# Kernel tuning notes

Hardware: AMD Instinct MI355X
Metric: run time of the kernel (lower is better)

The kernel has to match this reference:

```python
import jax, jax.numpy as jnp
import numpy as np

B, C, H, W = 8, 256, 128, 128
KC, VC, HEADS = 256, 256, 8


def setup_inputs() -> dict:
    key = jax.random.key(0)
    ks = jax.random.split(key, 10)
    s = 0.05
    return {
        "x": jax.random.normal(ks[0], (B, C, H, W), jnp.float32),
        "Wk": jax.random.normal(ks[1], (KC, C), jnp.float32) * s,
        "bk": jax.random.normal(ks[2], (KC,), jnp.float32) * s,
        "Wq": jax.random.normal(ks[3], (KC, C), jnp.float32) * s,
        "bq": jax.random.normal(ks[4], (KC,), jnp.float32) * s,
        "Wv": jax.random.normal(ks[5], (VC, C), jnp.float32) * s,
        "bv": jax.random.normal(ks[6], (VC,), jnp.float32) * s,
        "Wr": jax.random.normal(ks[7], (C, VC), jnp.float32) * s,
        "br": jax.random.normal(ks[8], (C,), jnp.float32) * s,
        "head_count": HEADS,
    }


def reference(x, Wk, bk, Wq, bq, Wv, bv, Wr, br, head_count):
    n, c, h, w = x.shape
    hw = h * w
    xf = x.reshape(n, c, hw)  # [n, C, S]
    # 1x1 convs == per-pixel linear projections
    keys = jnp.einsum('kc,ncs->nks', Wk, xf) + bk[None, :, None]
    queries = jnp.einsum('kc,ncs->nks', Wq, xf) + bq[None, :, None]
    values = jnp.einsum('vc,ncs->nvs', Wv, xf) + bv[None, :, None]

    dk = Wk.shape[0] // head_count
    dv = Wv.shape[0] // head_count
    # split heads along channel dim (matches torch channel slicing)
    K = jax.nn.softmax(keys.reshape(n, head_count, dk, hw), axis=-1)   # softmax over spatial
    Q = jax.nn.softmax(queries.reshape(n, head_count, dk, hw), axis=2) # softmax over key dim
    V = values.reshape(n, head_count, dv, hw)

    # context = K @ V^T : [n, h, dk, dv]
    ctx = jnp.einsum('nhks,nhvs->nhkv', K, V)
    # attended = ctx^T @ Q : [n, h, dv, S]
    att = jnp.einsum('nhkv,nhks->nhvs', ctx, Q).reshape(n, head_count * dv, h, w)

    attention = jnp.einsum('ov,nvhw->nohw', Wr, att) + br[None, :, None, None]
    # attention map: per-head mean over key dim, then mean over heads
    attention_map = K.mean(axis=2).mean(axis=1).reshape(n, h, w)
    # torch returns the LAST head's context (loop variable after the loop)
    context_last = ctx[:, -1]
    return attention, context_last, attention_map
```

## Files before the change

kernel.cpp:

```cpp
#include <hip/hip_runtime.h>
#include <hip/hip_bf16.h>

typedef float f32x4 __attribute__((ext_vector_type(4)));
typedef short s16x8 __attribute__((ext_vector_type(8)));
typedef short s16x4 __attribute__((ext_vector_type(4)));
typedef __bf16 bf16x8 __attribute__((ext_vector_type(8)));
typedef unsigned short u16;

#define DEVI __device__ __forceinline__

static constexpr int    HW      = 16384;
static constexpr size_t BSTRIDE = (size_t)256 * HW;

static constexpr size_t oXBT   = 0;
static constexpr size_t oEK    = oXBT  + (size_t)8 * HW * 256 * 2;
static constexpr size_t oQT    = oEK   + (size_t)8 * 256 * HW * 2;
static constexpr size_t oVB    = oQT   + (size_t)8 * HW * 256 * 2;
static constexpr size_t oWK    = oVB   + (size_t)8 * 256 * HW * 2;
static constexpr size_t oBIAS  = oWK   + (size_t)768 * 256 * 2;
static constexpr size_t oISE   = oBIAS + 4096;
static constexpr size_t oPS    = oISE  + 8192;
static constexpr size_t oCTX   = oPS   + (size_t)256 * 2048 * 4;
static constexpr size_t oMB    = oCTX  + (size_t)64 * 1024 * 4;
static constexpr size_t oCPART = oMB   + (size_t)8 * 256 * 256 * 2;
static constexpr size_t oMPART = oCPART + (size_t)4096 * 1024 * 4;

DEVI float bf2f(short x) {
  unsigned u = ((unsigned)(unsigned short)x) << 16;
  return __builtin_bit_cast(float, u);
}
DEVI u16 f2bf(float x) { return __builtin_bit_cast(u16, (__bf16)x); }

DEVI void gld16(const void* g, void* l) {
  __builtin_amdgcn_global_load_lds(
      (__attribute__((address_space(1))) void*)(g),
      (__attribute__((address_space(3))) void*)(l), 16, 0, 0);
}

DEVI void cfence() { asm volatile("" ::: "memory"); }

__global__ __launch_bounds__(256) void k_prep(
    const float* __restrict__ Wk, const float* __restrict__ Wq, const float* __restrict__ Wv,
    const float* __restrict__ bk, const float* __restrict__ bq, const float* __restrict__ bv,
    u16* __restrict__ Wkqv, float* __restrict__ bias)
{
  int i = blockIdx.x * 256 + threadIdx.x;
  for (int p = i; p < 768 * 256; p += 64 * 256) {
    float v = (p < 65536) ? Wk[p] : (p < 131072 ? Wq[p - 65536] : Wv[p - 131072]);
    Wkqv[p] = f2bf(v);
  }
  if (i < 768) bias[i] = (i < 256) ? bk[i] : (i < 512 ? bq[i - 256] : bv[i - 512]);
}

__global__ __launch_bounds__(256) void k_transpose(const float* __restrict__ in_, u16* __restrict__ out)
{
  __shared__ u16 lds[64 * 256];
  const int t = threadIdx.x;
  const int n = blockIdx.y;
  const int s0 = blockIdx.x * 64;
  const float* src = in_ + ((size_t)n * 256 + t) * HW + s0;
  #pragma unroll
  for (int i = 0; i < 16; ++i) {
    f32x4 v = *(const f32x4*)(src + i * 4);
    #pragma unroll
    for (int j = 0; j < 4; ++j) lds[(i * 4 + j) * 256 + t] = f2bf(v[j]);
  }
  __syncthreads();
  s16x8* gp = (s16x8*)(out + (size_t)n * BSTRIDE + (size_t)s0 * 256);
  const s16x8* lp = (const s16x8*)lds;
  #pragma unroll
  for (int i = 0; i < 8; ++i) gp[t + i * 256] = lp[t + i * 256];
}

template<int MODE>
__global__ __launch_bounds__(512, 2) void k_gemm256(
    const u16* __restrict__ A, const u16* __restrict__ B, const float* __restrict__ bias,
    u16* __restrict__ o_ek, u16* __restrict__ o_qT, u16* __restrict__ o_vb,
    float* __restrict__ o_ps, float* __restrict__ o_f32)
{
  __shared__ u16 smem[65536];
  const int t = threadIdx.x;
  const int L = blockIdx.x;
  const int n = L & 7;
  const int idx = L >> 3;
  int mb, sb;
  if constexpr (MODE == 0) { mb = idx % 3; sb = idx / 3; }
  else                     { mb = 0;       sb = idx; }
  const int s0 = sb * 256;
  const int lane = t & 63;
  const int l15 = lane & 15, l4 = lane >> 4;
  const int w = t >> 6;
  const int wr = w & 1, wc = w >> 1;
  const int tr = t >> 3;
  const int csw = (t & 7) ^ (tr & 7);

  const u16* Ag = A + (MODE == 0 ? (size_t)mb * 65536 : (size_t)n * 65536);
  const u16* Bg = B + (size_t)n * BSTRIDE + (size_t)s0 * 256;

  auto STAGE = [&](int buf, int kt) {
    const int k0 = kt * 64 + csw * 8;
    #pragma unroll
    for (int i = 0; i < 4; ++i) {
      const size_t r = (size_t)(i * 64 + tr);
      gld16(Ag + r * 256 + k0, smem + buf * 16384 + (i * 512 + t) * 8);
      gld16(Bg + r * 256 + k0, smem + 32768 + buf * 16384 + (i * 512 + t) * 8);
    }
  };

  f32x4 acc[8][4] = {};

  auto COMPUTE = [&](int buf) {
    const u16* Al = smem + buf * 16384;
    const u16* Bl = smem + 32768 + buf * 16384;
    bf16x8 bf[4][2];
    #pragma unroll
    for (int b = 0; b < 4; ++b) {
      const int s = wc * 64 + b * 16 + l15;
      #pragma unroll
      for (int ks = 0; ks < 2; ++ks)
        bf[b][ks] = *(const bf16x8*)&Bl[s * 64 + ((ks * 4 + l4) ^ (s & 7)) * 8];
    }
    #pragma unroll
    for (int p = 0; p < 4; ++p) {
      bf16x8 af[2][2];
      #pragma unroll
      for (int a2 = 0; a2 < 2; ++a2) {
        const int m = wr * 128 + (p * 2 + a2) * 16 + l15;
        #pragma unroll
        for (int ks = 0; ks < 2; ++ks)
          af[a2][ks] = *(const bf16x8*)&Al[m * 64 + ((ks * 4 + l4) ^ (m & 7)) * 8];
      }
      __builtin_amdgcn_s_setprio(1);
      #pragma unroll
      for (int a2 = 0; a2 < 2; ++a2)
        #pragma unroll
        for (int b = 0; b < 4; ++b)
          #pragma unroll
          for (int ks = 0; ks < 2; ++ks)
            acc[p * 2 + a2][b] = __builtin_amdgcn_mfma_f32_16x16x32_bf16(
                af[a2][ks], bf[b][ks], acc[p * 2 + a2][b], 0, 0, 0);
      __builtin_amdgcn_s_setprio(0);
    }
  };

  STAGE(0, 0); STAGE(1, 1);
  #pragma unroll
  for (int kt = 0; kt < 4; ++kt) {
    if (kt < 3) asm volatile("s_waitcnt vmcnt(8)" ::: "memory");
    else        asm volatile("s_waitcnt vmcnt(0)" ::: "memory");
    cfence(); __builtin_amdgcn_s_barrier(); cfence();
    COMPUTE(kt & 1);
    asm volatile("s_waitcnt lgkmcnt(0)" ::: "memory");
    cfence(); __builtin_amdgcn_s_barrier(); cfence();
    if (kt < 2) STAGE(kt & 1, kt + 2);
  }
  __syncthreads();

  if constexpr (MODE == 1) {
    float* O = o_f32 + (size_t)n * BSTRIDE;
    #pragma unroll
    for (int am = 0; am < 8; ++am)
      #pragma unroll
      for (int r = 0; r < 4; ++r) {
        const int m = wr * 128 + am * 16 + l4 * 4 + r;
        const float bb = bias[m];
        float* op = O + (size_t)m * HW + s0 + wc * 64 + l15;
        #pragma unroll
        for (int b = 0; b < 4; ++b) op[b * 16] = acc[am][b][r] + bb;
      }
    return;
  } else {
  if (mb == 0) {
    float* psrow = o_ps + ((size_t)(sb * 4 + wc) * 8 + n) * 256;
    u16* O = o_ek + (size_t)n * BSTRIDE;
    #pragma unroll
    for (int am = 0; am < 8; ++am)
      #pragma unroll
      for (int r = 0; r < 4; ++r) {
        const int m = wr * 128 + am * 16 + l4 * 4 + r;
        const float bb = bias[m];
        const float e0 = __expf(acc[am][0][r] + bb), e1 = __expf(acc[am][1][r] + bb);
        const float e2 = __expf(acc[am][2][r] + bb), e3 = __expf(acc[am][3][r] + bb);
        float s_ = e0 + e1 + e2 + e3;
        s_ += __shfl_xor(s_, 1); s_ += __shfl_xor(s_, 2);
        s_ += __shfl_xor(s_, 4); s_ += __shfl_xor(s_, 8);
        if (l15 == 0) psrow[m] = s_;
        u16* op = O + (size_t)m * HW + s0 + wc * 64 + l15;
        op[0] = f2bf(e0); op[16] = f2bf(e1); op[32] = f2bf(e2); op[48] = f2bf(e3);
      }
  } else if (mb == 1) {
    #pragma unroll
    for (int am = 0; am < 8; ++am)
      #pragma unroll
      for (int r = 0; r < 4; ++r) {
        const float bb = bias[256 + wr * 128 + am * 16 + l4 * 4 + r];
        #pragma unroll
        for (int b = 0; b < 4; ++b) acc[am][b][r] += bb;
      }
    #pragma unroll
    for (int hh = 0; hh < 4; ++hh)
      #pragma unroll
      for (int b = 0; b < 4; ++b) {
        float s = 0.f;
        #pragma unroll
        for (int a2 = 0; a2 < 2; ++a2)
          #pragma unroll
          for (int r = 0; r < 4; ++r) {
            const float e = __expf(acc[hh * 2 + a2][b][r]);
            acc[hh * 2 + a2][b][r] = e; s += e;
          }
        s += __shfl_xor(s, 16); s += __shfl_xor(s, 32);
        const float inv = 1.f / s;
        #pragma unroll
        for (int a2 = 0; a2 < 2; ++a2)
          #pragma unroll
          for (int r = 0; r < 4; ++r) acc[hh * 2 + a2][b][r] *= inv;
      }
    #pragma unroll
    for (int H = 0; H < 2; ++H) {
      if ((wc >> 1) == H) {
        #pragma unroll
        for (int am = 0; am < 8; ++am)
          #pragma unroll
          for (int b = 0; b < 4; ++b) {
            const int srow = wc * 64 + b * 16 + l15 - H * 128;
            s16x4 pk;
            #pragma unroll
            for (int r = 0; r < 4; ++r) pk[r] = (short)f2bf(acc[am][b][r]);
            *(s16x4*)&smem[srow * 264 + wr * 128 + am * 16 + l4 * 4] = pk;
          }
      }
      __syncthreads();
      const int row = t >> 2;
      const int cq = (t & 3) * 64;
      u16* dst = o_qT + (size_t)n * BSTRIDE + (size_t)(s0 + H * 128 + row) * 256 + cq;
      const u16* srcl = smem + row * 264 + cq;
      #pragma unroll
      for (int i = 0; i < 8; ++i) *(s16x8*)(dst + i * 8) = *(const s16x8*)(srcl + i * 8);
      __syncthreads();
    }
  } else {
    u16* O = o_vb + (size_t)n * BSTRIDE;
    #pragma unroll
    for (int am = 0; am < 8; ++am)
      #pragma unroll
      for (int r = 0; r < 4; ++r) {
        const int m = wr * 128 + am * 16 + l4 * 4 + r;
        const float bb = bias[512 + m];
        u16* op = O + (size_t)m * HW + s0 + wc * 64 + l15;
        #pragma unroll
        for (int b = 0; b < 4; ++b) op[b * 16] = f2bf(acc[am][b][r] + bb);
      }
  }
  }
}

__global__ __launch_bounds__(256) void k_inv(const float* __restrict__ ps, float* __restrict__ ise)
{
  const int i = blockIdx.x * 256 + threadIdx.x;
  float s = 0.f;
  for (int b = 0; b < 256; ++b) s += ps[(size_t)b * 2048 + i];
  ise[i] = 1.f / s;
}

__global__ __launch_bounds__(64) void k_ctx_part(
    const u16* __restrict__ ek, const u16* __restrict__ vb, const float* __restrict__ ise,
    float* __restrict__ cpart, float* __restrict__ mpart)
{
  const int blk = blockIdx.x;
  const int chunk = blk & 63, nh = blk >> 6;
  const int h = nh & 7, n = nh >> 3;
  const int lane = threadIdx.x;
  const int l15 = lane & 15, l4 = lane >> 4;
  const u16* kb = ek + ((size_t)n * 256 + h * 32) * HW;
  const u16* vv = vb + ((size_t)n * 256 + h * 32) * HW;
  const float iv0 = ise[n * 256 + h * 32 + l15];
  const float iv1 = ise[n * 256 + h * 32 + 16 + l15];
  f32x4 acc[2][2] = {};
  float macc[8][8] = {};
  const int sbase = chunk * 256 + l4 * 8;
  #pragma unroll
  for (int ks = 0; ks < 8; ++ks) {
    const int sb = sbase + ks * 32;
    bf16x8 ef[2], vf[2];
    #pragma unroll
    for (int g = 0; g < 2; ++g) {
      ef[g] = *(const bf16x8*)(kb + (size_t)(g * 16 + l15) * HW + sb);
      vf[g] = *(const bf16x8*)(vv + (size_t)(g * 16 + l15) * HW + sb);
    }
    #pragma unroll
    for (int j = 0; j < 8; ++j)
      macc[ks][j] = fmaf(iv0, (float)ef[0][j], fmaf(iv1, (float)ef[1][j], macc[ks][j]));
    #pragma unroll
    for (int a = 0; a < 2; ++a)
      #pragma unroll
      for (int b = 0; b < 2; ++b)
        acc[a][b] = __builtin_amdgcn_mfma_f32_16x16x32_bf16(ef[a], vf[b], acc[a][b], 0, 0, 0);
  }
  float* op = cpart + (size_t)blk * 1024;
  #pragma unroll
  for (int a = 0; a < 2; ++a)
    #pragma unroll
    for (int b = 0; b < 2; ++b)
      #pragma unroll
      for (int r = 0; r < 4; ++r)
        op[(a * 16 + l4 * 4 + r) * 32 + b * 16 + l15] = acc[a][b][r];
  #pragma unroll
  for (int ks = 0; ks < 8; ++ks)
    #pragma unroll
    for (int j = 0; j < 8; ++j) {
      float v = macc[ks][j];
      v += __shfl_xor(v, 1); v += __shfl_xor(v, 2);
      v += __shfl_xor(v, 4); v += __shfl_xor(v, 8);
      macc[ks][j] = v;
    }
  if (l15 == 0) {
    float* mp = mpart + ((size_t)h * 8 + n) * HW + sbase;
    #pragma unroll
    for (int ks = 0; ks < 8; ++ks) {
      f32x4 a = {macc[ks][0], macc[ks][1], macc[ks][2], macc[ks][3]};
      f32x4 b = {macc[ks][4], macc[ks][5], macc[ks][6], macc[ks][7]};
      *(f32x4*)(mp + ks * 32)     = a;
      *(f32x4*)(mp + ks * 32 + 4) = b;
    }
  }
}

__global__ __launch_bounds__(256) void k_ctx_reduce(
    const float* __restrict__ cpart, const float* __restrict__ ise,
    float* __restrict__ ctx, float* __restrict__ dctx)
{
  const int nh = blockIdx.x, n = nh >> 3, h = nh & 7, t = threadIdx.x;
  f32x4 a = {};
  for (int c = 0; c < 64; ++c) a += *(const f32x4*)(cpart + ((size_t)nh * 64 + c) * 1024 + t * 4);
  const float inv = ise[n * 256 + h * 32 + (t >> 3)];
  a *= inv;
  *(f32x4*)(ctx + (size_t)nh * 1024 + t * 4) = a;
  if (h == 7) *(f32x4*)(dctx + (size_t)n * 1024 + t * 4) = a;
}

__global__ __launch_bounds__(256) void k_mmat(
    const float* __restrict__ ctx, const float* __restrict__ Wr, u16* __restrict__ Mb)
{
  const int nh = blockIdx.x, n = nh >> 3, h = nh & 7, o = threadIdx.x;
  __shared__ float cl[1024];
  #pragma unroll
  for (int i = 0; i < 4; ++i) cl[o + i * 256] = ctx[(size_t)nh * 1024 + o + i * 256];
  __syncthreads();
  float wr[32];
  const float* wp = Wr + (size_t)o * 256 + h * 32;
  #pragma unroll
  for (int v = 0; v < 32; ++v) wr[v] = wp[v];
  u16* mp = Mb + ((size_t)n * 256 + o) * 256 + h * 32;
  #pragma unroll 4
  for (int k = 0; k < 32; ++k) {
    float s = 0.f;
    #pragma unroll
    for (int v = 0; v < 32; ++v) s += wr[v] * cl[k * 32 + v];
    mp[k] = f2bf(s);
  }
}

__global__ __launch_bounds__(256) void k_map_reduce(const float* __restrict__ mpart, float* __restrict__ dmap)
{
  const int i = blockIdx.x * 256 + threadIdx.x;
  f32x4 a = {};
  #pragma unroll
  for (int h = 0; h < 8; ++h) a += *(const f32x4*)(mpart + (size_t)h * 131072 + (size_t)i * 4);
  a *= (1.0f / 256.0f);
  *(f32x4*)(dmap + (size_t)i * 4) = a;
}

extern "C" void kernel_launch(void* const* d_in, const int* in_sizes, int n_in,
                              void* d_out, int out_size, void* d_ws, size_t ws_size,
                              hipStream_t stream)
{
  (void)in_sizes; (void)n_in; (void)out_size; (void)ws_size;
  const float* x  = (const float*)d_in[0];
  const float* Wk = (const float*)d_in[1];
  const float* bk = (const float*)d_in[2];
  const float* Wq = (const float*)d_in[3];
  const float* bq = (const float*)d_in[4];
  const float* Wv = (const float*)d_in[5];
  const float* bv = (const float*)d_in[6];
  const float* Wr = (const float*)d_in[7];
  const float* br = (const float*)d_in[8];

  char* ws = (char*)d_ws;
  u16*   xbT  = (u16*)(ws + oXBT);
  u16*   ek   = (u16*)(ws + oEK);
  u16*   qT   = (u16*)(ws + oQT);
  u16*   vb   = (u16*)(ws + oVB);
  u16*   Wkqv = (u16*)(ws + oWK);
  float* bias = (float*)(ws + oBIAS);
  float* ise  = (float*)(ws + oISE);
  float* ps   = (float*)(ws + oPS);
  float* ctx  = (float*)(ws + oCTX);
  u16*   Mb   = (u16*)(ws + oMB);
  float* cpart= (float*)(ws + oCPART);
  float* mpart= (float*)(ws + oMPART);

  float* attn = (float*)d_out;
  float* dctx = (float*)d_out + 33554432;
  float* dmap = (float*)d_out + 33562624;

  k_prep<<<64, 256, 0, stream>>>(Wk, Wq, Wv, bk, bq, bv, Wkqv, bias);
  k_transpose<<<dim3(256, 8), 256, 0, stream>>>(x, xbT);
  k_gemm256<0><<<1536, 512, 0, stream>>>(Wkqv, xbT, bias, ek, qT, vb, ps, nullptr);
  k_inv<<<8, 256, 0, stream>>>(ps, ise);
  k_ctx_part<<<4096, 64, 0, stream>>>(ek, vb, ise, cpart, mpart);
  k_ctx_reduce<<<64, 256, 0, stream>>>(cpart, ise, ctx, dctx);
  k_mmat<<<64, 256, 0, stream>>>(ctx, Wr, Mb);
  k_map_reduce<<<128, 256, 0, stream>>>(mpart, dmap);
  k_gemm256<1><<<512, 512, 0, stream>>>(Mb, qT, br, nullptr, nullptr, nullptr, nullptr, attn);
}
```

Baseline: 316.6 us.

## Restructure projection GEMMs to keep weights in registers and stream spatial tiles

The 256x256 GEMM kernel is replaced by a 256-thread variant in which each wave holds its 64 rows of the weight matrix entirely in registers. Only 64-pixel B tiles are streamed through double-buffered LDS, and the epilogue runs per tile. The swapped MFMA operand order lets the ek, vb and attention outputs be written as vectorized 4-element stores, and the qT output is written directly without an LDS transpose. The transpose kernel also gets a padded LDS layout with a different thread mapping. The cost is high register pressure from the 32 resident A fragments, plus complex vmcnt accounting.

Measured after the change: 377.1 us. +19.1%, slower.

```diff
diff --git a/kernel.cpp b/kernel.cpp
--- a/kernel.cpp
+++ b/kernel.cpp
@@ -37,8 +37,6 @@
       (__attribute__((address_space(3))) void*)(l), 16, 0, 0);
 }
 
-DEVI void cfence() { asm volatile("" ::: "memory"); }
-
 __global__ __launch_bounds__(256) void k_prep(
     const float* __restrict__ Wk, const float* __restrict__ Wq, const float* __restrict__ Wv,
     const float* __restrict__ bk, const float* __restrict__ bq, const float* __restrict__ bv,
@@ -52,206 +50,217 @@
   if (i < 768) bias[i] = (i < 256) ? bk[i] : (i < 512 ? bq[i - 256] : bv[i - 512]);
 }
 
-__global__ __launch_bounds__(256) void k_transpose(const float* __restrict__ in_, u16* __restrict__ out)
-{
-  __shared__ u16 lds[64 * 256];
+__global__ __launch_bounds__(256) void k_transpose(const float* __restrict__ x, u16* __restrict__ out)
+{
+  __shared__ u16 T[64 * 264];
   const int t = threadIdx.x;
   const int n = blockIdx.y;
   const int s0 = blockIdx.x * 64;
-  const float* src = in_ + ((size_t)n * 256 + t) * HW + s0;
+  const int cg = t >> 4;
+  const int sl = (t & 15) * 4;
   #pragma unroll
   for (int i = 0; i < 16; ++i) {
-    f32x4 v = *(const f32x4*)(src + i * 4);
-    #pragma unroll
-    for (int j = 0; j < 4; ++j) lds[(i * 4 + j) * 256 + t] = f2bf(v[j]);
+    const int c = i * 16 + cg;
+    f32x4 v = *(const f32x4*)(x + ((size_t)n * 256 + c) * HW + s0 + sl);
+    #pragma unroll
+    for (int j = 0; j < 4; ++j) T[(sl + j) * 264 + c] = f2bf(v[j]);
   }
   __syncthreads();
-  s16x8* gp = (s16x8*)(out + (size_t)n * BSTRIDE + (size_t)s0 * 256);
-  const s16x8* lp = (const s16x8*)lds;
-  #pragma unroll
-  for (int i = 0; i < 8; ++i) gp[t + i * 256] = lp[t + i * 256];
+  const int sr = t >> 2, ch = (t & 3) * 64;
+  u16* dst = out + (size_t)n * BSTRIDE + (size_t)(s0 + sr) * 256 + ch;
+  const u16* srcl = &T[sr * 264 + ch];
+  #pragma unroll
+  for (int i = 0; i < 8; ++i) *(s16x8*)(dst + i * 8) = *(const s16x8*)(srcl + i * 8);
 }
 
 template<int MODE>
-__global__ __launch_bounds__(512, 2) void k_gemm256(
+__global__ __launch_bounds__(256, 2) void k_gemmT(
     const u16* __restrict__ A, const u16* __restrict__ B, const float* __restrict__ bias,
     u16* __restrict__ o_ek, u16* __restrict__ o_qT, u16* __restrict__ o_vb,
     float* __restrict__ o_ps, float* __restrict__ o_f32)
 {
-  __shared__ u16 smem[65536];
+  __shared__ u16 smem[32768];
   const int t = threadIdx.x;
   const int L = blockIdx.x;
   const int n = L & 7;
-  const int idx = L >> 3;
-  int mb, sb;
-  if constexpr (MODE == 0) { mb = idx % 3; sb = idx / 3; }
-  else                     { mb = 0;       sb = idx; }
-  const int s0 = sb * 256;
+  int mb, sblock;
+  if constexpr (MODE == 0) { const int idx = L >> 3; mb = idx % 3; sblock = idx / 3; }
+  else                     { mb = 0; sblock = L >> 3; }
   const int lane = t & 63;
-  const int l15 = lane & 15, l4 = lane >> 4;
+  const int l15 = lane & 15, l4 = (lane >> 4) & 3;
   const int w = t >> 6;
-  const int wr = w & 1, wc = w >> 1;
-  const int tr = t >> 3;
-  const int csw = (t & 7) ^ (tr & 7);
-
-  const u16* Ag = A + (MODE == 0 ? (size_t)mb * 65536 : (size_t)n * 65536);
-  const u16* Bg = B + (size_t)n * BSTRIDE + (size_t)s0 * 256;
-
-  auto STAGE = [&](int buf, int kt) {
-    const int k0 = kt * 64 + csw * 8;
-    #pragma unroll
-    for (int i = 0; i < 4; ++i) {
-      const size_t r = (size_t)(i * 64 + tr);
-      gld16(Ag + r * 256 + k0, smem + buf * 16384 + (i * 512 + t) * 8);
-      gld16(Bg + r * 256 + k0, smem + 32768 + buf * 16384 + (i * 512 + t) * 8);
+  const bool sw = (MODE == 1) || (mb != 1);
+
+  const u16* Ag = (MODE == 0) ? A + (size_t)mb * 65536 : A + (size_t)n * 65536;
+  const u16* Bg = B + (size_t)n * BSTRIDE;
+
+  bf16x8 af[4][8];
+  #pragma unroll
+  for (int mf = 0; mf < 4; ++mf)
+    #pragma unroll
+    for (int kc = 0; kc < 8; ++kc)
+      af[mf][kc] = *(const bf16x8*)(Ag + (size_t)(w * 64 + mf * 16 + l15) * 256 + kc * 32 + l4 * 8);
+
+  float biasv[4];
+  f32x4 bq[4];
+  if constexpr (MODE == 0) {
+    if (mb != 1) {
+      const int bb = (mb == 0) ? 0 : 512;
+      #pragma unroll
+      for (int mf = 0; mf < 4; ++mf) biasv[mf] = bias[bb + w * 64 + mf * 16 + l15];
+    } else {
+      #pragma unroll
+      for (int mf = 0; mf < 4; ++mf)
+        #pragma unroll
+        for (int r = 0; r < 4; ++r) bq[mf][r] = bias[256 + w * 64 + mf * 16 + l4 * 4 + r];
+    }
+  } else {
+    #pragma unroll
+    for (int mf = 0; mf < 4; ++mf) biasv[mf] = bias[w * 64 + mf * 16 + l15];
+  }
+
+  const int rl_base = w * 16;
+  auto STAGE = [&](int buf, int tile) {
+    const int s0t = (sblock * 4 + tile) * 64;
+    #pragma unroll
+    for (int i = 0; i < 8; ++i) {
+      const int rl = rl_base + i * 2 + (lane >> 5);
+      const size_t gsrc = (size_t)(s0t + rl) * 256 + (size_t)(((lane & 31) ^ (rl & 7)) * 8);
+      gld16(Bg + gsrc, smem + buf * 16384 + (rl_base + i * 2) * 256);
     }
   };
 
-  f32x4 acc[8][4] = {};
-
-  auto COMPUTE = [&](int buf) {
-    const u16* Al = smem + buf * 16384;
-    const u16* Bl = smem + 32768 + buf * 16384;
-    bf16x8 bf[4][2];
-    #pragma unroll
-    for (int b = 0; b < 4; ++b) {
-      const int s = wc * 64 + b * 16 + l15;
-      #pragma unroll
-      for (int ks = 0; ks < 2; ++ks)
-        bf[b][ks] = *(const bf16x8*)&Bl[s * 64 + ((ks * 4 + l4) ^ (s & 7)) * 8];
-    }
-    #pragma unroll
-    for (int p = 0; p < 4; ++p) {
-      bf16x8 af[2][2];
-      #pragma unroll
-      for (int a2 = 0; a2 < 2; ++a2) {
-        const int m = wr * 128 + (p * 2 + a2) * 16 + l15;
-        #pragma unroll
-        for (int ks = 0; ks < 2; ++ks)
-          af[a2][ks] = *(const bf16x8*)&Al[m * 64 + ((ks * 4 + l4) ^ (m & 7)) * 8];
+  STAGE(0, 0);
+  STAGE(1, 1);
+
+  u16* ekb = o_ek + (size_t)n * BSTRIDE;
+  u16* vbb = o_vb + (size_t)n * BSTRIDE;
+  u16* qtb = o_qT + (size_t)n * BSTRIDE;
+  float* ob = o_f32 + (size_t)n * BSTRIDE;
+
+  #pragma unroll
+  for (int st = 0; st < 4; ++st) {
+    if (st == 0)      asm volatile("s_waitcnt vmcnt(8)" ::: "memory");
+    else if (st == 1) asm volatile("s_waitcnt vmcnt(24)" ::: "memory");
+    else if (st == 2) asm volatile("s_waitcnt vmcnt(40)" ::: "memory");
+    else              asm volatile("s_waitcnt vmcnt(32)" ::: "memory");
+    __builtin_amdgcn_s_barrier();
+
+    const int buf = st & 1;
+    const u16* Bl = smem + buf * 16384;
+    f32x4 acc[4][4] = {};
+
+    if (sw) {
+      #pragma unroll
+      for (int kc = 0; kc < 8; ++kc) {
+        bf16x8 bf[4];
+        #pragma unroll
+        for (int sf = 0; sf < 4; ++sf)
+          bf[sf] = *(const bf16x8*)&Bl[(sf * 16 + l15) * 256 + (((kc * 4 + l4) ^ (l15 & 7)) * 8)];
+        __builtin_amdgcn_s_setprio(1);
+        #pragma unroll
+        for (int sf = 0; sf < 4; ++sf)
+          #pragma unroll
+          for (int mf = 0; mf < 4; ++mf)
+            acc[sf][mf] = __builtin_amdgcn_mfma_f32_16x16x32_bf16(bf[sf], af[mf][kc], acc[sf][mf], 0, 0, 0);
+        __builtin_amdgcn_s_setprio(0);
       }
-      __builtin_amdgcn_s_setprio(1);
-      #pragma unroll
-      for (int a2 = 0; a2 < 2; ++a2)
-        #pragma unroll
-        for (int b = 0; b < 4; ++b)
-          #pragma unroll
-          for (int ks = 0; ks < 2; ++ks)
-            acc[p * 2 + a2][b] = __builtin_amdgcn_mfma_f32_16x16x32_bf16(
-                af[a2][ks], bf[b][ks], acc[p * 2 + a2][b], 0, 0, 0);
-      __builtin_amdgcn_s_setprio(0);
-    }
-  };
-
-  STAGE(0, 0); STAGE(1, 1);
-  #pragma unroll
-  for (int kt = 0; kt < 4; ++kt) {
-    if (kt < 3) asm volatile("s_waitcnt vmcnt(8)" ::: "memory");
-    else        asm volatile("s_waitcnt vmcnt(0)" ::: "memory");
-    cfence(); __builtin_amdgcn_s_barrier(); cfence();
-    COMPUTE(kt & 1);
+    } else {
+      #pragma unroll
+      for (int kc = 0; kc < 8; ++kc) {
+        bf16x8 bf[4];
+        #pragma unroll
+        for (int sf = 0; sf < 4; ++sf)
+          bf[sf] = *(const bf16x8*)&Bl[(sf * 16 + l15) * 256 + (((kc * 4 + l4) ^ (l15 & 7)) * 8)];
+        __builtin_amdgcn_s_setprio(1);
+        #pragma unroll
+        for (int mf = 0; mf < 4; ++mf)
+          #pragma unroll
+          for (int sf = 0; sf < 4; ++sf)
+            acc[mf][sf] = __builtin_amdgcn_mfma_f32_16x16x32_bf16(af[mf][kc], bf[sf], acc[mf][sf], 0, 0, 0);
+        __builtin_amdgcn_s_setprio(0);
+      }
+    }
+
     asm volatile("s_waitcnt lgkmcnt(0)" ::: "memory");
-    cfence(); __builtin_amdgcn_s_barrier(); cfence();
-    if (kt < 2) STAGE(kt & 1, kt + 2);
-  }
-  __syncthreads();
-
-  if constexpr (MODE == 1) {
-    float* O = o_f32 + (size_t)n * BSTRIDE;
-    #pragma unroll
-    for (int am = 0; am < 8; ++am)
-      #pragma unroll
-      for (int r = 0; r < 4; ++r) {
-        const int m = wr * 128 + am * 16 + l4 * 4 + r;
-        const float bb = bias[m];
-        float* op = O + (size_t)m * HW + s0 + wc * 64 + l15;
-        #pragma unroll
-        for (int b = 0; b < 4; ++b) op[b * 16] = acc[am][b][r] + bb;
+    __builtin_amdgcn_s_barrier();
+    if (st < 2) STAGE(buf, st + 2);
+
+    const int s0t = (sblock * 4 + st) * 64;
+    if constexpr (MODE == 1) {
+      #pragma unroll
+      for (int sf = 0; sf < 4; ++sf)
+        #pragma unroll
+        for (int mf = 0; mf < 4; ++mf) {
+          f32x4 o = acc[sf][mf] + biasv[mf];
+          __builtin_nontemporal_store(
+              o, (f32x4*)(ob + (size_t)(w * 64 + mf * 16 + l15) * HW + s0t + sf * 16 + l4 * 4));
+        }
+    } else if (mb == 0) {
+      float prow[4] = {0.f, 0.f, 0.f, 0.f};
+      #pragma unroll
+      for (int sf = 0; sf < 4; ++sf)
+        #pragma unroll
+        for (int mf = 0; mf < 4; ++mf) {
+          f32x4 e;
+          #pragma unroll
+          for (int r = 0; r < 4; ++r) e[r] = __expf(acc[sf][mf][r] + biasv[mf]);
+          prow[mf] += e[0] + e[1] + e[2] + e[3];
+          s16x4 pk;
+          #pragma unroll
+          for (int r = 0; r < 4; ++r) pk[r] = (short)f2bf(e[r]);
+          *(s16x4*)(ekb + (size_t)(w * 64 + mf * 16 + l15) * HW + s0t + sf * 16 + l4 * 4) = pk;
+        }
+      const int stile = sblock * 4 + st;
+      #pragma unroll
+      for (int mf = 0; mf < 4; ++mf) {
+        float v = prow[mf];
+        v += __shfl_xor(v, 16); v += __shfl_xor(v, 32);
+        prow[mf] = v;
       }
-    return;
-  } else {
-  if (mb == 0) {
-    float* psrow = o_ps + ((size_t)(sb * 4 + wc) * 8 + n) * 256;
-    u16* O = o_ek + (size_t)n * BSTRIDE;
-    #pragma unroll
-    for (int am = 0; am < 8; ++am)
-      #pragma unroll
-      for (int r = 0; r < 4; ++r) {
-        const int m = wr * 128 + am * 16 + l4 * 4 + r;
-        const float bb = bias[m];
-        const float e0 = __expf(acc[am][0][r] + bb), e1 = __expf(acc[am][1][r] + bb);
-        const float e2 = __expf(acc[am][2][r] + bb), e3 = __expf(acc[am][3][r] + bb);
-        float s_ = e0 + e1 + e2 + e3;
-        s_ += __shfl_xor(s_, 1); s_ += __shfl_xor(s_, 2);
-        s_ += __shfl_xor(s_, 4); s_ += __shfl_xor(s_, 8);
-        if (l15 == 0) psrow[m] = s_;
-        u16* op = O + (size_t)m * HW + s0 + wc * 64 + l15;
-        op[0] = f2bf(e0); op[16] = f2bf(e1); op[32] = f2bf(e2); op[48] = f2bf(e3);
+      if (l4 == 0) {
+        #pragma unroll
+        for (int mf = 0; mf < 4; ++mf)
+          o_ps[(size_t)stile * 2048 + n * 256 + w * 64 + mf * 16 + l15] = prow[mf];
       }
-  } else if (mb == 1) {
-    #pragma unroll
-    for (int am = 0; am < 8; ++am)
-      #pragma unroll
-      for (int r = 0; r < 4; ++r) {
-        const float bb = bias[256 + wr * 128 + am * 16 + l4 * 4 + r];
-        #pragma unroll
-        for (int b = 0; b < 4; ++b) acc[am][b][r] += bb;
+    } else if (mb == 1) {
+      #pragma unroll
+      for (int mf = 0; mf < 4; ++mf)
+        #pragma unroll
+        for (int sf = 0; sf < 4; ++sf)
+          #pragma unroll
+          for (int r = 0; r < 4; ++r) acc[mf][sf][r] = __expf(acc[mf][sf][r] + bq[mf][r]);
+      #pragma unroll
+      for (int sf = 0; sf < 4; ++sf) {
+        float h0 = 0.f, h1 = 0.f;
+        #pragma unroll
+        for (int r = 0; r < 4; ++r) {
+          h0 += acc[0][sf][r] + acc[1][sf][r];
+          h1 += acc[2][sf][r] + acc[3][sf][r];
+        }
+        h0 += __shfl_xor(h0, 16); h0 += __shfl_xor(h0, 32);
+        h1 += __shfl_xor(h1, 16); h1 += __shfl_xor(h1, 32);
+        const float i0 = 1.f / h0, i1 = 1.f / h1;
+        #pragma unroll
+        for (int mf = 0; mf < 4; ++mf) {
+          const float iv = (mf < 2) ? i0 : i1;
+          s16x4 pk;
+          #pragma unroll
+          for (int r = 0; r < 4; ++r) pk[r] = (short)f2bf(acc[mf][sf][r] * iv);
+          *(s16x4*)(qtb + (size_t)(s0t + sf * 16 + l15) * 256 + w * 64 + mf * 16 + l4 * 4) = pk;
+        }
       }
-    #pragma unroll
-    for (int hh = 0; hh < 4; ++hh)
-      #pragma unroll
-      for (int b = 0; b < 4; ++b) {
-        float s = 0.f;
-        #pragma unroll
-        for (int a2 = 0; a2 < 2; ++a2)
-          #pragma unroll
-          for (int r = 0; r < 4; ++r) {
-            const float e = __expf(acc[hh * 2 + a2][b][r]);
-            acc[hh * 2 + a2][b][r] = e; s += e;
-          }
-        s += __shfl_xor(s, 16); s += __shfl_xor(s, 32);
-        const float inv = 1.f / s;
-        #pragma unroll
-        for (int a2 = 0; a2 < 2; ++a2)
-          #pragma unroll
-          for (int r = 0; r < 4; ++r) acc[hh * 2 + a2][b][r] *= inv;
-      }
-    #pragma unroll
-    for (int H = 0; H < 2; ++H) {
-      if ((wc >> 1) == H) {
-        #pragma unroll
-        for (int am = 0; am < 8; ++am)
-          #pragma unroll
-          for (int b = 0; b < 4; ++b) {
-            const int srow = wc * 64 + b * 16 + l15 - H * 128;
-            s16x4 pk;
-            #pragma unroll
-            for (int r = 0; r < 4; ++r) pk[r] = (short)f2bf(acc[am][b][r]);
-            *(s16x4*)&smem[srow * 264 + wr * 128 + am * 16 + l4 * 4] = pk;
-          }
-      }
-      __syncthreads();
-      const int row = t >> 2;
-      const int cq = (t & 3) * 64;
-      u16* dst = o_qT + (size_t)n * BSTRIDE + (size_t)(s0 + H * 128 + row) * 256 + cq;
-      const u16* srcl = smem + row * 264 + cq;
-      #pragma unroll
-      for (int i = 0; i < 8; ++i) *(s16x8*)(dst + i * 8) = *(const s16x8*)(srcl + i * 8);
-      __syncthreads();
-    }
-  } else {
-    u16* O = o_vb + (size_t)n * BSTRIDE;
-    #pragma unroll
-    for (int am = 0; am < 8; ++am)
-      #pragma unroll
-      for (int r = 0; r < 4; ++r) {
-        const int m = wr * 128 + am * 16 + l4 * 4 + r;
-        const float bb = bias[512 + m];
-        u16* op = O + (size_t)m * HW + s0 + wc * 64 + l15;
-        #pragma unroll
-        for (int b = 0; b < 4; ++b) op[b * 16] = f2bf(acc[am][b][r] + bb);
-      }
-  }
+    } else {
+      #pragma unroll
+      for (int sf = 0; sf < 4; ++sf)
+        #pragma unroll
+        for (int mf = 0; mf < 4; ++mf) {
+          s16x4 pk;
+          #pragma unroll
+          for (int r = 0; r < 4; ++r) pk[r] = (short)f2bf(acc[sf][mf][r] + biasv[mf]);
+          *(s16x4*)(vbb + (size_t)(w * 64 + mf * 16 + l15) * HW + s0t + sf * 16 + l4 * 4) = pk;
+        }
+    }
   }
 }
 
@@ -406,11 +415,11 @@
 
   k_prep<<<64, 256, 0, stream>>>(Wk, Wq, Wv, bk, bq, bv, Wkqv, bias);
   k_transpose<<<dim3(256, 8), 256, 0, stream>>>(x, xbT);
-  k_gemm256<0><<<1536, 512, 0, stream>>>(Wkqv, xbT, bias, ek, qT, vb, ps, nullptr);
+  k_gemmT<0><<<1536, 256, 0, stream>>>(Wkqv, xbT, bias, ek, qT, vb, ps, nullptr);
   k_inv<<<8, 256, 0, stream>>>(ps, ise);
   k_ctx_part<<<4096, 64, 0, stream>>>(ek, vb, ise, cpart, mpart);
   k_ctx_reduce<<<64, 256, 0, stream>>>(cpart, ise, ctx, dctx);
   k_mmat<<<64, 256, 0, stream>>>(ctx, Wr, Mb);
   k_map_reduce<<<128, 256, 0, stream>>>(mpart, dmap);
-  k_gemm256<1><<<512, 512, 0, stream>>>(Mb, qT, br, nullptr, nullptr, nullptr, nullptr, attn);
-}
+  k_gemmT<1><<<512, 256, 0, stream>>>(Mb, qT, br, nullptr, nullptr, nullptr, nullptr, attn);
+}
```
